# Kernel optimization log

Measured on AMD Instinct MI355X. Metric: run time of the kernel, lower is better.

## Reference

```python
import jax, jax.numpy as jnp
import numpy as np

B, C, U = 8, 32, 32
K = 5            # powers = k + 1 with k = 4
N1, N2 = 256, 256


def setup_inputs() -> dict:
    key = jax.random.key(0)
    k_x, k_c1, k_c2, k_w = jax.random.split(key, 4)
    x = jax.random.normal(k_x, (B, C, N1, N2), dtype=jnp.float32)
    # Chebyshev polynomial bases T_0..T_k of the (rescaled) Laplacians of the
    # two factor graphs; registered buffers in the torch module.
    cheb1 = jax.random.normal(k_c1, (K, N1, N1), dtype=jnp.float32)
    cheb2 = jax.random.normal(k_c2, (K, N2, N2), dtype=jnp.float32)
    # Trainable anisotropic coefficients [powers, powers, channels, units],
    # initialized N(0, 0.001) in the original module.
    coefs = jax.random.normal(k_w, (K, K, C, U), dtype=jnp.float32) * 0.001
    return {"x": x, "cheb1": cheb1, "cheb2": cheb2, "coefs": coefs}


def reference(x, cheb1, cheb2, coefs):
    """Fused form of the anisotropic Chebyshev convolution.

    Original triple loop computes
      out[b,u,m,n] = sum_{k1,k2,i,p,q}
          coefs[k1,k2,i,u] * cheb1[k1,p,m] * cheb2[k2,q,n] * x[b,i,p,q]
    """
    # Filter along the first graph axis for every power k1: [B, K, C, N1, N2]
    a = jnp.einsum('kpm,bipq->bkimq', cheb1, x)
    # Contract channels and k1 with the learned coefficients: [B, K, U, N1, N2]
    c = jnp.einsum('bkimq,kliu->blumq', a, coefs)
    # Filter along the second graph axis for every power k2: [B, U, N1, N2]
    out = jnp.einsum('blumq,lqn->bumn', c, cheb2)
    return out
```

## Files before the change

kernel.cpp:

```cpp
#include <hip/hip_runtime.h>
#include <stdint.h>

#define WB 8
#define WC 32
#define WU 32
#define WK 5
#define WN 256
#define NN 65536
#define KC 160
#define KQ 1280

typedef __attribute__((ext_vector_type(8))) short bf8;
typedef __attribute__((ext_vector_type(8))) unsigned short us8;
typedef __attribute__((ext_vector_type(4))) float f4;

__device__ __forceinline__ unsigned short f2b(float f) {
    union { float f; uint32_t u; } v; v.f = f;
    uint32_t u = v.u;
    return (unsigned short)((u + 0x7FFFu + ((u >> 16) & 1u)) >> 16);
}

__device__ __forceinline__ void gload16(const unsigned short* g, unsigned short* l) {
    __builtin_amdgcn_global_load_lds(
        (const __attribute__((address_space(1))) unsigned int*)g,
        (__attribute__((address_space(3))) unsigned int*)l, 16, 0, 0);
}

__global__ void prep_small(const float* __restrict__ cheb1,
                           const float* __restrict__ cheb2,
                           const float* __restrict__ coefs,
                           unsigned short* __restrict__ c1T,
                           unsigned short* __restrict__ c2T,
                           unsigned short* __restrict__ Wt) {
    int idx = blockIdx.x * 256 + threadIdx.x;
    if (idx < WK * NN) {
        int k = idx / NN, r = idx % NN, m = r / WN, p = r % WN;
        c1T[idx] = f2b(cheb1[(k * WN + p) * WN + m]);
    }
    if (idx < WN * KQ) {
        int n = idx / KQ, r = idx % KQ;
        c2T[idx] = f2b(cheb2[r * WN + n]);
    }
    if (idx < KC * KC) {
        int lu = idx / KC, ki = idx % KC;
        int l = lu >> 5, u = lu & 31, k = ki >> 5, i = ki & 31;
        Wt[idx] = f2b(coefs[((k * WK + l) * WC + i) * WU + u]);
    }
}

__global__ void prep_x(const float* __restrict__ x, unsigned short* __restrict__ xT) {
    __shared__ unsigned short tile[64][72];
    int bi = blockIdx.z;
    int p0 = blockIdx.y * 64, q0 = blockIdx.x * 64;
    const float* src = x + (size_t)bi * NN;
    unsigned short* dst = xT + (size_t)bi * NN;
    int t = threadIdx.x;
    int c4 = (t & 15) * 4, r0 = t >> 4;
    for (int it = 0; it < 4; ++it) {
        int r = r0 + it * 16;
        float4 v = *reinterpret_cast<const float4*>(&src[(size_t)(p0 + r) * WN + q0 + c4]);
        tile[r][c4 + 0] = f2b(v.x); tile[r][c4 + 1] = f2b(v.y);
        tile[r][c4 + 2] = f2b(v.z); tile[r][c4 + 3] = f2b(v.w);
    }
    __syncthreads();
    for (int it = 0; it < 4; ++it) {
        int q = r0 + it * 16;
        ushort4 o;
        o.x = tile[c4 + 0][q]; o.y = tile[c4 + 1][q];
        o.z = tile[c4 + 2][q]; o.w = tile[c4 + 3][q];
        *reinterpret_cast<ushort4*>(&dst[(size_t)(q0 + q) * WN + p0 + c4]) = o;
    }
}

__global__ __launch_bounds__(512, 4) void g1(const unsigned short* __restrict__ c1T,
                                             const unsigned short* __restrict__ xT,
                                             unsigned short* __restrict__ a, int b_base) {
    __shared__ unsigned short As[128 * 64];
    __shared__ unsigned short Bs[256 * 64];
    int z = blockIdx.y;
    int bl = z >> 5, i = z & 31;
    int row0 = blockIdx.x * 128;
    int b = b_base + bl;
    const unsigned short* Asrc = c1T;
    const unsigned short* Bsrc = xT + (size_t)(b * WC + i) * NN;
    unsigned short* Out = a + (size_t)bl * KC * NN;

    int t = threadIdx.x;
    int w = t >> 6, l = t & 63;
    int wm = (w >> 2) * 64, wn = (w & 3) * 64;
    int lr = l & 15, hi = l >> 4;
    int srow = l >> 3;
    int scol = ((l & 7) ^ srow) * 8;

    f4 acc[4][4];
    for (int mf = 0; mf < 4; ++mf) for (int nf = 0; nf < 4; ++nf) acc[mf][nf] = (f4)(0.0f);

    for (int p0 = 0; p0 < 256; p0 += 64) {
        __syncthreads();
        for (int it = 0; it < 2; ++it) {
            int chunk = it * 8 + w;
            int row = chunk * 8 + srow;
            gload16(&Asrc[(size_t)(row0 + row) * 256 + p0 + scol], &As[chunk * 512]);
        }
        for (int it = 0; it < 4; ++it) {
            int chunk = it * 8 + w;
            int row = chunk * 8 + srow;
            gload16(&Bsrc[(size_t)row * 256 + p0 + scol], &Bs[chunk * 512]);
        }
        __syncthreads();
        for (int kk = 0; kk < 2; ++kk) {
            bf8 af[4], bfr[4];
            for (int mf = 0; mf < 4; ++mf) {
                int r = wm + mf * 16 + lr;
                af[mf] = *(const bf8*)&As[r * 64 + (((kk * 4 + hi) ^ (r & 7)) * 8)];
            }
            for (int nf = 0; nf < 4; ++nf) {
                int rb = wn + nf * 16 + lr;
                bfr[nf] = *(const bf8*)&Bs[rb * 64 + (((kk * 4 + hi) ^ (rb & 7)) * 8)];
            }
            for (int mf = 0; mf < 4; ++mf)
                for (int nf = 0; nf < 4; ++nf)
                    acc[mf][nf] = __builtin_amdgcn_mfma_f32_16x16x32_bf16(af[mf], bfr[nf], acc[mf][nf], 0, 0, 0);
        }
    }
    for (int mf = 0; mf < 4; ++mf)
        for (int nf = 0; nf < 4; ++nf)
            for (int j = 0; j < 4; ++j) {
                int grow = row0 + wm + mf * 16 + hi * 4 + j;
                int k = grow >> 8, m = grow & 255;
                int q = wn + nf * 16 + lr;
                Out[(size_t)(k * 32 + i) * NN + m * 256 + q] = f2b(acc[mf][nf][j]);
            }
}

__global__ __launch_bounds__(512, 4) void g2p(const unsigned short* __restrict__ Wt,
                                              const unsigned short* __restrict__ a,
                                              unsigned short* __restrict__ c) {
    __shared__ unsigned short Bt[128 * 172];
    int bl = blockIdx.y;
    int n0 = blockIdx.x * 128;
    const unsigned short* asrc = a + (size_t)bl * KC * NN;
    unsigned short* Out = c + (size_t)bl * KC * NN;
    int t = threadIdx.x;

    for (int s = 0; s < 2; ++s) {
        int task = t + s * 512;
        if (task < 640) {
            int oct = task & 15, kq = task >> 4;
            const unsigned short* src = asrc + (size_t)(kq * 4) * NN + n0 + oct * 8;
            us8 v0 = *(const us8*)&src[0 * NN];
            us8 v1 = *(const us8*)&src[1 * NN];
            us8 v2 = *(const us8*)&src[2 * NN];
            us8 v3 = *(const us8*)&src[3 * NN];
            #pragma unroll
            for (int j = 0; j < 8; ++j) {
                ushort4 wv;
                wv.x = v0[j]; wv.y = v1[j]; wv.z = v2[j]; wv.w = v3[j];
                *reinterpret_cast<ushort4*>(&Bt[(oct * 8 + j) * 172 + kq * 4]) = wv;
            }
        }
    }
    __syncthreads();

    int w = t >> 6, l = t & 63;
    int mh = w >> 2, nq = w & 3;
    int lr = l & 15, hi = l >> 4;
    f4 acc[5][2];
    for (int mf = 0; mf < 5; ++mf) { acc[mf][0] = (f4)(0.0f); acc[mf][1] = (f4)(0.0f); }

    for (int kk = 0; kk < 5; ++kk) {
        int k0 = kk * 32 + hi * 8;
        bf8 bfr[2];
        #pragma unroll
        for (int nf = 0; nf < 2; ++nf) {
            int pix = (nq * 2 + nf) * 16 + lr;
            typedef __attribute__((ext_vector_type(4))) short s4v;
            s4v lo  = *(const s4v*)&Bt[pix * 172 + k0];
            s4v hi4 = *(const s4v*)&Bt[pix * 172 + k0 + 4];
            bfr[nf] = __builtin_shufflevector(lo, hi4, 0, 1, 2, 3, 4, 5, 6, 7);
        }
        #pragma unroll
        for (int mf = 0; mf < 5; ++mf) {
            int row = mh * 80 + mf * 16 + lr;
            bf8 afr = *(const bf8*)&Wt[(size_t)row * KC + k0];
            acc[mf][0] = __builtin_amdgcn_mfma_f32_16x16x32_bf16(afr, bfr[0], acc[mf][0], 0, 0, 0);
            acc[mf][1] = __builtin_amdgcn_mfma_f32_16x16x32_bf16(afr, bfr[1], acc[mf][1], 0, 0, 0);
        }
    }
    for (int mf = 0; mf < 5; ++mf)
        for (int nf = 0; nf < 2; ++nf)
            for (int j = 0; j < 4; ++j) {
                int row = mh * 80 + mf * 16 + hi * 4 + j;
                int col = n0 + (nq * 2 + nf) * 16 + lr;
                Out[(size_t)row * NN + col] = f2b(acc[mf][nf][j]);
            }
}

__global__ __launch_bounds__(512, 4) void g3(const unsigned short* __restrict__ c,
                                             const unsigned short* __restrict__ c2T,
                                             float* __restrict__ out, int b_base) {
    __shared__ unsigned short As[128 * 64];
    __shared__ unsigned short Bs[256 * 64];
    int bl = blockIdx.y;
    int b = b_base + bl;
    int R0 = blockIdx.x * 128;
    int u = R0 >> 8, m0 = R0 & 255;
    const unsigned short* Csrc = c + (size_t)bl * KC * NN;

    int t = threadIdx.x;
    int w = t >> 6, l = t & 63;
    int wm = (w >> 2) * 64, wn = (w & 3) * 64;
    int lr = l & 15, hi = l >> 4;
    int srow = l >> 3;
    int scol = ((l & 7) ^ srow) * 8;

    f4 acc[4][4];
    for (int mf = 0; mf < 4; ++mf) for (int nf = 0; nf < 4; ++nf) acc[mf][nf] = (f4)(0.0f);

    for (int step = 0; step < 20; ++step) {
        int lq = step >> 2, q0 = (step & 3) * 64;
        const unsigned short* Arow0 = Csrc + (size_t)(lq * 32 + u) * NN + (size_t)m0 * 256 + q0;
        const unsigned short* Brow0 = c2T + step * 64;
        __syncthreads();
        for (int it = 0; it < 2; ++it) {
            int chunk = it * 8 + w;
            int row = chunk * 8 + srow;
            gload16(&Arow0[(size_t)row * 256 + scol], &As[chunk * 512]);
        }
        for (int it = 0; it < 4; ++it) {
            int chunk = it * 8 + w;
            int row = chunk * 8 + srow;
            gload16(&Brow0[(size_t)row * KQ + scol], &Bs[chunk * 512]);
        }
        __syncthreads();
        for (int kk = 0; kk < 2; ++kk) {
            bf8 af[4], bfr[4];
            for (int mf = 0; mf < 4; ++mf) {
                int r = wm + mf * 16 + lr;
                af[mf] = *(const bf8*)&As[r * 64 + (((kk * 4 + hi) ^ (r & 7)) * 8)];
            }
            for (int nf = 0; nf < 4; ++nf) {
                int rb = wn + nf * 16 + lr;
                bfr[nf] = *(const bf8*)&Bs[rb * 64 + (((kk * 4 + hi) ^ (rb & 7)) * 8)];
            }
            for (int mf = 0; mf < 4; ++mf)
                for (int nf = 0; nf < 4; ++nf)
                    acc[mf][nf] = __builtin_amdgcn_mfma_f32_16x16x32_bf16(af[mf], bfr[nf], acc[mf][nf], 0, 0, 0);
        }
    }
    for (int mf = 0; mf < 4; ++mf)
        for (int nf = 0; nf < 4; ++nf)
            for (int j = 0; j < 4; ++j) {
                int m = m0 + wm + mf * 16 + hi * 4 + j;
                int n = wn + nf * 16 + lr;
                out[((size_t)(b * WU + u) * WN + m) * WN + n] = acc[mf][nf][j];
            }
}

extern "C" void kernel_launch(void* const* d_in, const int* in_sizes, int n_in,
                              void* d_out, int out_size, void* d_ws, size_t ws_size,
                              hipStream_t stream) {
    const float* x     = (const float*)d_in[0];
    const float* cheb1 = (const float*)d_in[1];
    const float* cheb2 = (const float*)d_in[2];
    const float* coefs = (const float*)d_in[3];
    float* out = (float*)d_out;
    unsigned short* ws = (unsigned short*)d_ws;

    size_t off = 0;
    unsigned short* xT  = ws + off; off += (size_t)WB * WC * NN;
    unsigned short* c1T = ws + off; off += (size_t)WK * NN;
    unsigned short* c2T = ws + off; off += (size_t)WN * KQ;
    unsigned short* Wt  = ws + off; off += (size_t)KC * KC;
    size_t fixed_elems = off;
    size_t a1 = (size_t)KC * NN;

    prep_small<<<1280, 256, 0, stream>>>(cheb1, cheb2, coefs, c1T, c2T, Wt);
    prep_x<<<dim3(4, 4, WB * WC), 256, 0, stream>>>(x, xT);

    size_t avail = ws_size / 2;
    size_t rem = avail > fixed_elems ? avail - fixed_elems : 0;

    if (rem >= 9 * a1) {
        int nb = (int)((rem - 8 * a1) / a1);
        if (nb < 1) nb = 1;
        if (nb > WB) nb = WB;
        unsigned short* a_ = ws + fixed_elems;
        unsigned short* c_ = a_ + (size_t)nb * a1;
        for (int b0 = 0; b0 < WB; b0 += nb) {
            int cur = (WB - b0 < nb) ? (WB - b0) : nb;
            g1<<<dim3(10, cur * 32), 512, 0, stream>>>(c1T, xT, a_, b0);
            g2p<<<dim3(512, cur), 512, 0, stream>>>(Wt, a_, c_ + (size_t)b0 * a1);
        }
        g3<<<dim3(64, WB), 512, 0, stream>>>(c_, c2T, out, 0);
    } else {
        size_t per_b = 2 * a1;
        int nb = (int)(rem / per_b);
        if (nb < 1) nb = 1;
        if (nb > WB) nb = WB;
        unsigned short* a_ = ws + fixed_elems;
        unsigned short* c_ = a_ + (size_t)nb * a1;
        for (int b0 = 0; b0 < WB; b0 += nb) {
            int cur = (WB - b0 < nb) ? (WB - b0) : nb;
            g1<<<dim3(10, cur * 32), 512, 0, stream>>>(c1T, xT, a_, b0);
            g2p<<<dim3(512, cur), 512, 0, stream>>>(Wt, a_, c_);
            g3<<<dim3(64, cur), 512, 0, stream>>>(c_, c2T, out, b0);
        }
    }
}
```

Before: 283.7 us.

## Triple-buffer A tiles in g3 and load B fragments directly from global

The g3 GEMM kernel now prefetches the next A tile into a three-slot LDS ring with async global-to-LDS loads, using an explicit vmcnt wait and a single barrier per step instead of two syncthreads. B fragments (c2T) are read straight from global memory into registers rather than staged through LDS. The launch-bounds occupancy hint drops from 4 to 2. The intent is to overlap memory latency with MFMA work and cut LDS traffic and barriers. The trade-offs are more register pressure and uncoalesced, repeated global reads of B. The hand-tuned vmcnt counts are fragile because they depend on how many loads the compiler issues.

```diff
diff --git a/kernel.cpp b/kernel.cpp
--- a/kernel.cpp
+++ b/kernel.cpp
@@ -196,11 +196,10 @@
             }
 }
 
-__global__ __launch_bounds__(512, 4) void g3(const unsigned short* __restrict__ c,
+__global__ __launch_bounds__(512, 2) void g3(const unsigned short* __restrict__ c,
                                              const unsigned short* __restrict__ c2T,
                                              float* __restrict__ out, int b_base) {
-    __shared__ unsigned short As[128 * 64];
-    __shared__ unsigned short Bs[256 * 64];
+    __shared__ unsigned short As[3][128 * 64];
     int bl = blockIdx.y;
     int b = b_base + bl;
     int R0 = blockIdx.x * 128;
@@ -217,37 +216,47 @@
     f4 acc[4][4];
     for (int mf = 0; mf < 4; ++mf) for (int nf = 0; nf < 4; ++nf) acc[mf][nf] = (f4)(0.0f);
 
+#define G3_STAGE_A(buf, step) do { \
+    int lq_ = (step) >> 2, q0_ = ((step) & 3) * 64; \
+    const unsigned short* Arow0 = Csrc + (size_t)(lq_ * 32 + u) * NN + (size_t)m0 * 256 + q0_; \
+    for (int it = 0; it < 2; ++it) { \
+        int chunk = it * 8 + w; int row = chunk * 8 + srow; \
+        gload16(&Arow0[(size_t)row * 256 + scol], &As[buf][chunk * 512]); } \
+} while (0)
+
+    G3_STAGE_A(0, 0);
     for (int step = 0; step < 20; ++step) {
-        int lq = step >> 2, q0 = (step & 3) * 64;
-        const unsigned short* Arow0 = Csrc + (size_t)(lq * 32 + u) * NN + (size_t)m0 * 256 + q0;
-        const unsigned short* Brow0 = c2T + step * 64;
-        __syncthreads();
-        for (int it = 0; it < 2; ++it) {
-            int chunk = it * 8 + w;
-            int row = chunk * 8 + srow;
-            gload16(&Arow0[(size_t)row * 256 + scol], &As[chunk * 512]);
-        }
-        for (int it = 0; it < 4; ++it) {
-            int chunk = it * 8 + w;
-            int row = chunk * 8 + srow;
-            gload16(&Brow0[(size_t)row * KQ + scol], &Bs[chunk * 512]);
-        }
-        __syncthreads();
+        int cur = step % 3;
+        bf8 bfr[2][4];
+        #pragma unroll
+        for (int kk = 0; kk < 2; ++kk)
+            #pragma unroll
+            for (int nf = 0; nf < 4; ++nf) {
+                int rb = wn + nf * 16 + lr;
+                bfr[kk][nf] = *(const bf8*)&c2T[(size_t)rb * KQ + step * 64 + (kk * 4 + hi) * 8];
+            }
+        if (step < 19) {
+            G3_STAGE_A((step + 1) % 3, step + 1);
+            asm volatile("s_waitcnt vmcnt(10)" ::: "memory");
+        } else {
+            asm volatile("s_waitcnt vmcnt(8)" ::: "memory");
+        }
+        __builtin_amdgcn_s_barrier();
+        asm volatile("" ::: "memory");
         for (int kk = 0; kk < 2; ++kk) {
-            bf8 af[4], bfr[4];
+            bf8 af[4];
+            #pragma unroll
             for (int mf = 0; mf < 4; ++mf) {
                 int r = wm + mf * 16 + lr;
-                af[mf] = *(const bf8*)&As[r * 64 + (((kk * 4 + hi) ^ (r & 7)) * 8)];
-            }
-            for (int nf = 0; nf < 4; ++nf) {
-                int rb = wn + nf * 16 + lr;
-                bfr[nf] = *(const bf8*)&Bs[rb * 64 + (((kk * 4 + hi) ^ (rb & 7)) * 8)];
+                af[mf] = *(const bf8*)&As[cur][r * 64 + (((kk * 4 + hi) ^ (r & 7)) * 8)];
             }
             for (int mf = 0; mf < 4; ++mf)
                 for (int nf = 0; nf < 4; ++nf)
-                    acc[mf][nf] = __builtin_amdgcn_mfma_f32_16x16x32_bf16(af[mf], bfr[nf], acc[mf][nf], 0, 0, 0);
-        }
-    }
+                    acc[mf][nf] = __builtin_amdgcn_mfma_f32_16x16x32_bf16(af[mf], bfr[kk][nf], acc[mf][nf], 0, 0, 0);
+        }
+        asm volatile("" ::: "memory");
+    }
+#undef G3_STAGE_A
     for (int mf = 0; mf < 4; ++mf)
         for (int nf = 0; nf < 4; ++nf)
             for (int j = 0; j < 4; ++j) {
```

Result: slower. 330.1 us (+16.4%).
